# Performance work log

Measured on AMD Instinct MI355X. Metric: run time of the kernel, lower is better.

## Reference

```python
import jax, jax.numpy as jnp
from jax import lax
import numpy as np
import math

MAXV = 127.0  # 2**(8-1)-1, signed int8 narrow range

def setup_inputs() -> dict:
    key = jax.random.key(0)
    kx, kw, kb = jax.random.split(key, 3)
    B, Cin, H, W = 32, 128, 56, 56
    Cout, K = 256, 3
    x = jax.random.normal(kx, (B, Cin, H, W), dtype=jnp.float32)
    # kaiming_uniform_(a=sqrt(5)) -> bound = sqrt(6 / ((1+5) * fan_in)) = 1/sqrt(fan_in)
    fan_in = Cin * K * K
    bound = 1.0 / math.sqrt(fan_in)
    weight = jax.random.uniform(kw, (Cout, Cin, K, K), dtype=jnp.float32,
                                minval=-bound, maxval=bound)
    bias = jax.random.uniform(kb, (Cout,), dtype=jnp.float32,
                              minval=-bound, maxval=bound)
    return {"x": x, "weight": weight, "bias": bias}

def _quantize_i8(t):
    """Max-calibrated signed 8-bit quantization (fake_quant=False -> integer output)."""
    amax = jnp.max(jnp.abs(t))
    scale = MAXV / amax
    q = jnp.clip(jnp.round(t * scale), -MAXV, MAXV).astype(jnp.int8)
    return q, scale

def reference(x, weight, bias):
    # quantize activations and weights to int8
    qx, sx = _quantize_i8(x)
    qw, sw = _quantize_i8(weight)
    # exact int8 conv with int32 accumulation (systolic exact path), stride=1, pad=1
    out_i32 = lax.conv_general_dilated(
        qx, qw,
        window_strides=(1, 1),
        padding=((1, 1), (1, 1)),
        dimension_numbers=("NCHW", "OIHW", "NCHW"),
        preferred_element_type=jnp.int32,
    )
    # dequantize and add bias
    out = out_i32.astype(jnp.float32) / (sx * sw)
    return out + bias[None, :, None, None]
```

## Files before the change

kernel.cpp:

```cpp
#include <hip/hip_runtime.h>


#define B_    32
#define CIN   128
#define H_    56
#define W_    56
#define COUT  256
#define HP    58
#define WP    58
#define HWP   (H_*W_)
#define NPIX  (B_*HWP)
#define NCHUNK 18
#define ACHUNK 16384

typedef int int4v __attribute__((ext_vector_type(4)));

__device__ __forceinline__ void gld_lds16(const void* g, void* l) {
    __builtin_amdgcn_global_load_lds(
        (const __attribute__((address_space(1))) unsigned int*)g,
        (__attribute__((address_space(3))) unsigned int*)l, 16, 0, 0);
}

__global__ __launch_bounds__(256) void amax_kernel(const float4* __restrict__ x, long n4x,
                                                   const float4* __restrict__ wt, long n4w,
                                                   unsigned* __restrict__ scales) {
    const float4* p; long n4; unsigned* slot; long start, stride;
    if (blockIdx.x < 2048) {
        p = x; n4 = n4x; slot = scales;
        start = (long)blockIdx.x * 256 + threadIdx.x; stride = 2048L * 256;
    } else {
        p = wt; n4 = n4w; slot = scales + 1;
        start = (long)(blockIdx.x - 2048) * 256 + threadIdx.x; stride = 128L * 256;
    }
    float m = 0.f;
    for (long i = start; i < n4; i += stride) {
        float4 v = p[i];
        m = fmaxf(m, fmaxf(fmaxf(fabsf(v.x), fabsf(v.y)), fmaxf(fabsf(v.z), fabsf(v.w))));
    }
    __shared__ float red[256];
    red[threadIdx.x] = m; __syncthreads();
    for (int s = 128; s > 0; s >>= 1) {
        if (threadIdx.x < s) red[threadIdx.x] = fmaxf(red[threadIdx.x], red[threadIdx.x + s]);
        __syncthreads();
    }
    if (threadIdx.x == 0) atomicMax(slot, __float_as_uint(red[0]));
}

__global__ __launch_bounds__(256) void quant_x_kernel(const float* __restrict__ x,
        const unsigned* __restrict__ scales, signed char* __restrict__ xq) {
    const int bh = blockIdx.x;
    const int b = bh / H_, h = bh % H_;
    const float sx = 127.0f / __uint_as_float(scales[0]);
    __shared__ int ldsq[W_ * 33];
    const int tid = threadIdx.x;

    int4 z; z.x = 0; z.y = 0; z.z = 0; z.w = 0;
    int4* prow = (int4*)(xq + ((long)b * HP + h + 1) * WP * CIN);
    if (tid < 8) prow[tid] = z;
    else if (tid < 16) prow[456 + tid - 8] = z;
    if (h == 0) {
        int4* r0 = (int4*)(xq + (long)b * HP * WP * CIN);
        for (int i = tid; i < 464; i += 256) r0[i] = z;
    } else if (h == H_ - 1) {
        int4* rt = (int4*)(xq + ((long)b * HP + 57) * WP * CIN);
        for (int i = tid; i < 464; i += 256) rt[i] = z;
    }

    const int w = tid & 63;
    const int chi = tid >> 6;
    if (w < W_) {
        const float* xb = x + (long)b * CIN * HWP + h * W_ + w;
#pragma unroll
        for (int it = 0; it < 8; ++it) {
            const int c4 = it * 4 + chi;
            int pk = 0;
#pragma unroll
            for (int u = 0; u < 4; ++u) {
                float v = xb[(long)(c4 * 4 + u) * HWP];
                float q = fminf(127.f, fmaxf(-127.f, rintf(v * sx)));
                pk |= ((int)q & 0xff) << (u * 8);
            }
            ldsq[w * 33 + c4] = pk;
        }
    }
    __syncthreads();
    int4* dst = (int4*)(xq + (((long)b * HP + h + 1) * WP + 1) * CIN);
    for (int idx = tid; idx < W_ * 8; idx += 256) {
        const int ww = idx >> 3, c16 = idx & 7;
        int4 v;
        v.x = ldsq[ww * 33 + c16 * 4 + 0];
        v.y = ldsq[ww * 33 + c16 * 4 + 1];
        v.z = ldsq[ww * 33 + c16 * 4 + 2];
        v.w = ldsq[ww * 33 + c16 * 4 + 3];
        dst[ww * 8 + c16] = v;
    }
}

__global__ __launch_bounds__(256) void quant_w_kernel(const float* __restrict__ wt,
        const unsigned* __restrict__ scales, signed char* __restrict__ wq) {
    const int id = blockIdx.x * 256 + threadIdx.x;
    if (id >= COUT * 9 * 32) return;
    const float sw = 127.0f / __uint_as_float(scales[1]);
    const int co = id / 288;
    const int r  = id % 288;
    const int t  = r / 32;
    const int c4 = r % 32;
    int pk = 0;
#pragma unroll
    for (int u = 0; u < 4; ++u) {
        float v = wt[(co * CIN + c4 * 4 + u) * 9 + t];
        float q = fminf(127.f, fmaxf(-127.f, rintf(v * sw)));
        pk |= ((int)q & 0xff) << (u * 8);
    }
    const int k = t * CIN + c4 * 4;
    const int chunk = k >> 6;
    const int off = k & 63;
    *(int*)(wq + (long)chunk * ACHUNK + (off >> 4) * 4096 + co * 16 + (off & 15)) = pk;
}

__global__ __launch_bounds__(512, 4) void conv_kernel(
        const signed char* __restrict__ xq, const signed char* __restrict__ wq,
        const float* __restrict__ bias, const unsigned* __restrict__ scales,
        float* __restrict__ out) {
    __shared__ signed char smem[73728];

    const int tid = threadIdx.x;
    const int lane = tid & 63;
    const int wv = tid >> 6;
    const int ln = lane & 15;
    const int g  = lane >> 4;

    const int wco = wv >> 1;
    const int wpx = wv & 1;

    const int bid = blockIdx.x;
    const int wg  = (bid & 7) * 98 + (bid >> 3);
    const int px_blk = wg * 128;

    const int aoff0 = wv * 2048 + lane * 16;
    const int aoff1 = aoff0 + 1024;

    const int gB = wv >> 1, halfB = wv & 1;
    const int pxs = px_blk + halfB * 64 + lane;
    const int bS = pxs / HWP, hwS = pxs % HWP;
    const int hS = hwS / W_, wS = hwS % W_;
    const signed char* srcB = xq + ((bS * HP + hS) * WP + wS) * CIN + gB * 16;
    const int ldsB = gB * 2048 + halfB * 1024 + lane * 16;

#define STAGE(c) { \
    const int tap_ = (c) >> 1; \
    const int toff_ = ((tap_ / 3) * WP + (tap_ % 3)) * CIN + ((c) & 1) * 64; \
    const int bf_ = (c) % 3; \
    gld_lds16(wq + (c) * ACHUNK + aoff0, &smem[bf_ * 16384 + aoff0]); \
    gld_lds16(wq + (c) * ACHUNK + aoff1, &smem[bf_ * 16384 + aoff1]); \
    gld_lds16(srcB + toff_, &smem[49152 + bf_ * 8192 + ldsB]); }

#define LDA_(i) (*(const int4v*)&smem[buf * 16384 + g * 4096 + (wco * 64 + (i) * 16 + ln) * 16])
#define LDB_(j) (*(const int4v*)&smem[49152 + buf * 8192 + g * 2048 + (wpx * 64 + (j) * 16 + ln) * 16])
#define MM(i, j, A, Bv) acc[i][j] = __builtin_amdgcn_mfma_i32_16x16x64_i8(A, Bv, acc[i][j], 0, 0, 0)

#define CHUNK(c, VM) { \
    const int buf = (c) % 3; \
    asm volatile("s_waitcnt vmcnt(" #VM ")\n\ts_barrier" ::: "memory"); \
    if ((c) + 2 < NCHUNK) STAGE((c) + 2); \
    int4v Bf0 = LDB_(0), Bf1 = LDB_(1), Bf2 = LDB_(2), Bf3 = LDB_(3); \
    int4v Af0 = LDA_(0), Af1 = LDA_(1), Af2 = LDA_(2), Af3 = LDA_(3); \
    __builtin_amdgcn_s_setprio(1); \
    MM(0, 0, Af0, Bf0); MM(0, 1, Af0, Bf1); MM(0, 2, Af0, Bf2); MM(0, 3, Af0, Bf3); \
    MM(1, 0, Af1, Bf0); MM(1, 1, Af1, Bf1); MM(1, 2, Af1, Bf2); MM(1, 3, Af1, Bf3); \
    MM(2, 0, Af2, Bf0); MM(2, 1, Af2, Bf1); MM(2, 2, Af2, Bf2); MM(2, 3, Af2, Bf3); \
    MM(3, 0, Af3, Bf0); MM(3, 1, Af3, Bf1); MM(3, 2, Af3, Bf2); MM(3, 3, Af3, Bf3); \
    __builtin_amdgcn_s_setprio(0); }

    int4v acc[4][4] = {};
    STAGE(0);
    STAGE(1);
    CHUNK(0, 3)  CHUNK(1, 3)  CHUNK(2, 3)  CHUNK(3, 3)  CHUNK(4, 3)  CHUNK(5, 3)
    CHUNK(6, 3)  CHUNK(7, 3)  CHUNK(8, 3)  CHUNK(9, 3)  CHUNK(10, 3) CHUNK(11, 3)
    CHUNK(12, 3) CHUNK(13, 3) CHUNK(14, 3) CHUNK(15, 3) CHUNK(16, 3) CHUNK(17, 0)
#undef CHUNK
#undef MM
#undef LDA_
#undef LDB_
#undef STAGE

    const float ax = __uint_as_float(scales[0]);
    const float aw = __uint_as_float(scales[1]);
    const float inv = 1.0f / ((127.0f / ax) * (127.0f / aw));

    __syncthreads();
    float* ldsT = (float*)smem;

    const int c4 = tid & 31;
    const int rsel = tid >> 5;
    const int px4 = px_blk + c4 * 4;
    const int bb = px4 / HWP, hw = px4 - bb * HWP;
    float4* outb = (float4*)(out + (long)bb * COUT * HWP + hw);

#pragma unroll
    for (int p = 0; p < 2; ++p) {
        if ((wv >> 2) == p) {
            const int cl0 = (wco & 1) * 64;
#pragma unroll
            for (int i = 0; i < 4; ++i)
#pragma unroll
                for (int r = 0; r < 4; ++r) {
                    const int cl = cl0 + i * 16 + g * 4 + r;
#pragma unroll
                    for (int j = 0; j < 4; ++j)
                        ldsT[cl * 130 + wpx * 64 + j * 16 + ln] = (float)acc[i][j][r] * inv;
                }
        }
        __syncthreads();
#pragma unroll
        for (int it = 0; it < 8; ++it) {
            const int row = it * 16 + rsel;
            const int co = p * 128 + row;
            float4 v = *(float4*)&ldsT[row * 130 + c4 * 4];
            const float bsv = bias[co];
            v.x += bsv; v.y += bsv; v.z += bsv; v.w += bsv;
            outb[(long)co * (HWP / 4)] = v;
        }
        if (p == 0) __syncthreads();
    }
}

extern "C" void kernel_launch(void* const* d_in, const int* in_sizes, int n_in,
                              void* d_out, int out_size, void* d_ws, size_t ws_size,
                              hipStream_t stream) {
    const float* x  = (const float*)d_in[0];
    const float* wt = (const float*)d_in[1];
    const float* bs = (const float*)d_in[2];
    float* out = (float*)d_out;

    unsigned* scales = (unsigned*)d_ws;
    const size_t XQ_OFF   = 256;
    const size_t XQ_BYTES = (size_t)B_ * HP * WP * CIN;
    signed char* xq = (signed char*)d_ws + XQ_OFF;
    signed char* wq = xq + XQ_BYTES;

    hipMemsetAsync(d_ws, 0, 8, stream);

    const long n4x = (long)B_ * CIN * H_ * W_ / 4;
    const long n4w = (long)COUT * CIN * 9 / 4;
    amax_kernel<<<2176, 256, 0, stream>>>((const float4*)x, n4x, (const float4*)wt, n4w, scales);

    quant_x_kernel<<<B_ * H_, 256, 0, stream>>>(x, scales, xq);
    quant_w_kernel<<<(COUT * 9 * 32 + 255) / 256, 256, 0, stream>>>(wt, scales, wq);

    conv_kernel<<<NPIX / 128, 512, 0, stream>>>(xq, wq, bs, scales, out);
}
```

Baseline: 214.5 us.

## Split conv tile by output-channel halves and load activations directly into registers

The conv kernel now uses 256-thread blocks that each handle 128 pixels by 128 output channels, so twice as many blocks cover the two channel halves. Weight chunks still go through a triple-buffered LDS staging path, but the weight layout is reorganised per 128-channel half. Activation fragments are now loaded straight from global memory into registers and double-buffered there, instead of being staged through LDS. This shrinks LDS use to 24 KB per block for higher occupancy and removes the LDS round trip for activations, at the cost of redundant activation reads across the two channel halves and more register pressure.

```diff
diff --git a/kernel.cpp b/kernel.cpp
--- a/kernel.cpp
+++ b/kernel.cpp
@@ -11,7 +11,7 @@
 #define HWP   (H_*W_)
 #define NPIX  (B_*HWP)
 #define NCHUNK 18
-#define ACHUNK 16384
+#define WCHUNK 16384
 
 typedef int int4v __attribute__((ext_vector_type(4)));
 
@@ -114,15 +114,16 @@
     }
     const int k = t * CIN + c4 * 4;
     const int chunk = k >> 6;
-    const int off = k & 63;
-    *(int*)(wq + (long)chunk * ACHUNK + (off >> 4) * 4096 + co * 16 + (off & 15)) = pk;
-}
-
-__global__ __launch_bounds__(512, 4) void conv_kernel(
+    const int o = k & 63;
+    *(int*)(wq + (long)chunk * WCHUNK + (co >> 7) * 8192 +
+            (o >> 4) * 2048 + (co & 127) * 16 + (o & 15)) = pk;
+}
+
+__global__ __launch_bounds__(256, 3) void conv_kernel(
         const signed char* __restrict__ xq, const signed char* __restrict__ wq,
         const float* __restrict__ bias, const unsigned* __restrict__ scales,
         float* __restrict__ out) {
-    __shared__ signed char smem[73728];
+    __shared__ signed char smem[24576];
 
     const int tid = threadIdx.x;
     const int lane = tid & 63;
@@ -130,59 +131,72 @@
     const int ln = lane & 15;
     const int g  = lane >> 4;
 
-    const int wco = wv >> 1;
-    const int wpx = wv & 1;
+    const int wco2 = wv >> 1;
+    const int wpx2 = wv & 1;
 
     const int bid = blockIdx.x;
-    const int wg  = (bid & 7) * 98 + (bid >> 3);
-    const int px_blk = wg * 128;
-
-    const int aoff0 = wv * 2048 + lane * 16;
-    const int aoff1 = aoff0 + 1024;
-
-    const int gB = wv >> 1, halfB = wv & 1;
-    const int pxs = px_blk + halfB * 64 + lane;
-    const int bS = pxs / HWP, hwS = pxs % HWP;
-    const int hS = hwS / W_, wS = hwS % W_;
-    const signed char* srcB = xq + ((bS * HP + hS) * WP + wS) * CIN + gB * 16;
-    const int ldsB = gB * 2048 + halfB * 1024 + lane * 16;
-
-#define STAGE(c) { \
-    const int tap_ = (c) >> 1; \
-    const int toff_ = ((tap_ / 3) * WP + (tap_ % 3)) * CIN + ((c) & 1) * 64; \
-    const int bf_ = (c) % 3; \
-    gld_lds16(wq + (c) * ACHUNK + aoff0, &smem[bf_ * 16384 + aoff0]); \
-    gld_lds16(wq + (c) * ACHUNK + aoff1, &smem[bf_ * 16384 + aoff1]); \
-    gld_lds16(srcB + toff_, &smem[49152 + bf_ * 8192 + ldsB]); }
-
-#define LDA_(i) (*(const int4v*)&smem[buf * 16384 + g * 4096 + (wco * 64 + (i) * 16 + ln) * 16])
-#define LDB_(j) (*(const int4v*)&smem[49152 + buf * 8192 + g * 2048 + (wpx * 64 + (j) * 16 + ln) * 16])
+    const int wg  = (bid & 7) * 196 + (bid >> 3);
+    const int pxt = wg >> 1;
+    const int cot = wg & 1;
+    const int px_blk = pxt * 128;
+    const int cotoff = cot * 8192;
+
+    const int aoff0 = wv * 1024 + lane * 16;
+    const int aoff1 = aoff0 + 4096;
+
+    int voff[4];
+#pragma unroll
+    for (int j = 0; j < 4; ++j) {
+        const int pxs = px_blk + wpx2 * 64 + j * 16 + ln;
+        const int bS = pxs / HWP, hwS = pxs % HWP;
+        const int hS = hwS / W_, wS = hwS % W_;
+        voff[j] = ((bS * HP + hS) * WP + wS) * CIN + g * 16;
+    }
+    const int voff0 = voff[0], voff1 = voff[1], voff2 = voff[2], voff3 = voff[3];
+
+#define STAGE_A(c) { const int bf_ = (c) % 3; \
+    gld_lds16(wq + (c) * WCHUNK + cotoff + aoff0, &smem[bf_ * 8192 + aoff0]); \
+    gld_lds16(wq + (c) * WCHUNK + cotoff + aoff1, &smem[bf_ * 8192 + aoff1]); }
+
+#define LOADB(c, BN) { const int tap_ = (c) >> 1; \
+    const signed char* p_ = xq + ((tap_ / 3) * WP + (tap_ % 3)) * CIN + ((c) & 1) * 64; \
+    BN##0 = *(const int4v*)(p_ + voff0); BN##1 = *(const int4v*)(p_ + voff1); \
+    BN##2 = *(const int4v*)(p_ + voff2); BN##3 = *(const int4v*)(p_ + voff3); }
+
+#define LDA_(i) (*(const int4v*)&smem[buf * 8192 + g * 2048 + (wco2 * 64 + (i) * 16 + ln) * 16])
 #define MM(i, j, A, Bv) acc[i][j] = __builtin_amdgcn_mfma_i32_16x16x64_i8(A, Bv, acc[i][j], 0, 0, 0)
 
-#define CHUNK(c, VM) { \
+#define CHUNK(c, VM, BC, BN) { \
     const int buf = (c) % 3; \
     asm volatile("s_waitcnt vmcnt(" #VM ")\n\ts_barrier" ::: "memory"); \
-    if ((c) + 2 < NCHUNK) STAGE((c) + 2); \
-    int4v Bf0 = LDB_(0), Bf1 = LDB_(1), Bf2 = LDB_(2), Bf3 = LDB_(3); \
+    if ((c) + 2 < NCHUNK) STAGE_A((c) + 2); \
+    __builtin_amdgcn_sched_barrier(0);   \
+    if ((c) + 1 < NCHUNK) LOADB((c) + 1, BN); \
     int4v Af0 = LDA_(0), Af1 = LDA_(1), Af2 = LDA_(2), Af3 = LDA_(3); \
     __builtin_amdgcn_s_setprio(1); \
-    MM(0, 0, Af0, Bf0); MM(0, 1, Af0, Bf1); MM(0, 2, Af0, Bf2); MM(0, 3, Af0, Bf3); \
-    MM(1, 0, Af1, Bf0); MM(1, 1, Af1, Bf1); MM(1, 2, Af1, Bf2); MM(1, 3, Af1, Bf3); \
-    MM(2, 0, Af2, Bf0); MM(2, 1, Af2, Bf1); MM(2, 2, Af2, Bf2); MM(2, 3, Af2, Bf3); \
-    MM(3, 0, Af3, Bf0); MM(3, 1, Af3, Bf1); MM(3, 2, Af3, Bf2); MM(3, 3, Af3, Bf3); \
+    MM(0, 0, Af0, BC##0); MM(0, 1, Af0, BC##1); MM(0, 2, Af0, BC##2); MM(0, 3, Af0, BC##3); \
+    MM(1, 0, Af1, BC##0); MM(1, 1, Af1, BC##1); MM(1, 2, Af1, BC##2); MM(1, 3, Af1, BC##3); \
+    MM(2, 0, Af2, BC##0); MM(2, 1, Af2, BC##1); MM(2, 2, Af2, BC##2); MM(2, 3, Af2, BC##3); \
+    MM(3, 0, Af3, BC##0); MM(3, 1, Af3, BC##1); MM(3, 2, Af3, BC##2); MM(3, 3, Af3, BC##3); \
     __builtin_amdgcn_s_setprio(0); }
 
     int4v acc[4][4] = {};
-    STAGE(0);
-    STAGE(1);
-    CHUNK(0, 3)  CHUNK(1, 3)  CHUNK(2, 3)  CHUNK(3, 3)  CHUNK(4, 3)  CHUNK(5, 3)
-    CHUNK(6, 3)  CHUNK(7, 3)  CHUNK(8, 3)  CHUNK(9, 3)  CHUNK(10, 3) CHUNK(11, 3)
-    CHUNK(12, 3) CHUNK(13, 3) CHUNK(14, 3) CHUNK(15, 3) CHUNK(16, 3) CHUNK(17, 0)
+    int4v Ba0, Ba1, Ba2, Ba3, Bb0, Bb1, Bb2, Bb3;
+    STAGE_A(0);
+    __builtin_amdgcn_sched_barrier(0);
+    STAGE_A(1);
+    __builtin_amdgcn_sched_barrier(0);
+    LOADB(0, Ba);
+    CHUNK(0,  6, Ba, Bb) CHUNK(1,  6, Bb, Ba) CHUNK(2,  6, Ba, Bb) CHUNK(3,  6, Bb, Ba)
+    CHUNK(4,  6, Ba, Bb) CHUNK(5,  6, Bb, Ba) CHUNK(6,  6, Ba, Bb) CHUNK(7,  6, Bb, Ba)
+    CHUNK(8,  6, Ba, Bb) CHUNK(9,  6, Bb, Ba) CHUNK(10, 6, Ba, Bb) CHUNK(11, 6, Bb, Ba)
+    CHUNK(12, 6, Ba, Bb) CHUNK(13, 6, Bb, Ba) CHUNK(14, 6, Ba, Bb) CHUNK(15, 6, Bb, Ba)
+    CHUNK(16, 6, Ba, Bb) CHUNK(17, 4, Bb, Ba)
 #undef CHUNK
 #undef MM
 #undef LDA_
-#undef LDB_
-#undef STAGE
+#undef LOADB
+#undef STAGE_A
 
     const float ax = __uint_as_float(scales[0]);
     const float aw = __uint_as_float(scales[1]);
@@ -195,33 +209,34 @@
     const int rsel = tid >> 5;
     const int px4 = px_blk + c4 * 4;
     const int bb = px4 / HWP, hw = px4 - bb * HWP;
-    float4* outb = (float4*)(out + (long)bb * COUT * HWP + hw);
-
-#pragma unroll
-    for (int p = 0; p < 2; ++p) {
-        if ((wv >> 2) == p) {
-            const int cl0 = (wco & 1) * 64;
-#pragma unroll
-            for (int i = 0; i < 4; ++i)
+    float* outb = out + ((long)bb * COUT + cot * 128) * HWP + hw;
+
+#pragma unroll
+    for (int rnd = 0; rnd < 4; ++rnd) {
+        if (wco2 == (rnd >> 1)) {
+#pragma unroll
+            for (int ii = 0; ii < 2; ++ii) {
+                const int i = (rnd & 1) * 2 + ii;
 #pragma unroll
                 for (int r = 0; r < 4; ++r) {
-                    const int cl = cl0 + i * 16 + g * 4 + r;
+                    const int cl = ii * 16 + g * 4 + r;
 #pragma unroll
                     for (int j = 0; j < 4; ++j)
-                        ldsT[cl * 130 + wpx * 64 + j * 16 + ln] = (float)acc[i][j][r] * inv;
+                        ldsT[cl * 130 + wpx2 * 64 + j * 16 + ln] = (float)acc[i][j][r] * inv;
                 }
+            }
         }
         __syncthreads();
 #pragma unroll
-        for (int it = 0; it < 8; ++it) {
-            const int row = it * 16 + rsel;
-            const int co = p * 128 + row;
+        for (int rr = 0; rr < 4; ++rr) {
+            const int row = rr * 8 + rsel;
+            const int co = rnd * 32 + row;
             float4 v = *(float4*)&ldsT[row * 130 + c4 * 4];
-            const float bsv = bias[co];
+            const float bsv = bias[cot * 128 + co];
             v.x += bsv; v.y += bsv; v.z += bsv; v.w += bsv;
-            outb[(long)co * (HWP / 4)] = v;
+            *(float4*)&outb[(long)co * HWP] = v;
         }
-        if (p == 0) __syncthreads();
+        if (rnd < 3) __syncthreads();
     }
 }
 
@@ -248,5 +263,5 @@
     quant_x_kernel<<<B_ * H_, 256, 0, stream>>>(x, scales, xq);
     quant_w_kernel<<<(COUT * 9 * 32 + 255) / 256, 256, 0, stream>>>(wt, scales, wq);
 
-    conv_kernel<<<NPIX / 128, 512, 0, stream>>>(xq, wq, bs, scales, out);
-}
+    conv_kernel<<<2 * NPIX / 128, 256, 0, stream>>>(xq, wq, bs, scales, out);
+}
```

Result: slower. 240.6 us (+12.1%).
